# Kernel optimization log

Hardware: AMD Instinct MI355X
Metric: run time of the kernel (lower is better)

## Reference

```python
import jax, jax.numpy as jnp
import numpy as np

N_NODES = 50000


def gcn_conv(x, W, b, src, dst, num_nodes):
    """PyG GCNConv: add self-loops, symmetric deg^{-1/2} normalization,
    linear transform, scatter-add aggregation, bias."""
    loop = jnp.arange(num_nodes, dtype=src.dtype)
    s = jnp.concatenate([src, loop])  # message sources
    d = jnp.concatenate([dst, loop])  # message destinations
    deg = jax.ops.segment_sum(jnp.ones_like(d, dtype=x.dtype), d, num_segments=num_nodes)
    dinv = jnp.where(deg > 0, jax.lax.rsqrt(deg), 0.0)
    norm = dinv[s] * dinv[d]                      # [E+N]
    h = x @ W                                      # [N, out]
    msg = h[s] * norm[:, None]                     # gather + scale  [E+N, out]
    out = jax.ops.segment_sum(msg, d, num_segments=num_nodes)  # scatter-add
    return out + b


def setup_inputs() -> dict:
    key = jax.random.key(0)
    ks = jax.random.split(key, 8)
    n, e = N_NODES, 1600000
    d_in, d_h, d_out = 128, 128, 64
    x = jax.random.normal(ks[0], (n, d_in), dtype=jnp.float32)
    edge_index = jax.random.randint(ks[1], (2, e), 0, n, dtype=jnp.int32)
    s = 1.0 / np.sqrt(d_in)
    W1 = jax.random.uniform(ks[2], (d_in, d_h), jnp.float32, -s, s)
    b1 = jnp.zeros((d_h,), jnp.float32)
    W2 = jax.random.uniform(ks[3], (d_h, d_h), jnp.float32, -s, s)
    b2 = jnp.zeros((d_h,), jnp.float32)
    W3 = jax.random.uniform(ks[4], (d_h, d_out), jnp.float32, -s, s)
    b3 = jnp.zeros((d_out,), jnp.float32)
    return {"x": x, "edge_index": edge_index, "W1": W1, "b1": b1,
            "W2": W2, "b2": b2, "W3": W3, "b3": b3}


def reference(x, edge_index, W1, b1, W2, b2, W3, b3):
    src, dst = edge_index[0], edge_index[1]
    n = x.shape[0]
    # Dropout in eval mode (identity); ReLU between GCN layers.
    h = jax.nn.relu(gcn_conv(x, W1, b1, src, dst, n))
    h = jax.nn.relu(gcn_conv(h, W2, b2, src, dst, n))
    out = gcn_conv(h, W3, b3, src, dst, n)
    return out
```

## Files before the change

### kernel.cpp

```cpp
#include <hip/hip_runtime.h>
#include <type_traits>


#define EPB  4096
#define DIRW 197

typedef __attribute__((ext_vector_type(8))) short bf16x8;
typedef __attribute__((ext_vector_type(4))) float f32x4;
typedef __attribute__((ext_vector_type(2))) float f32x2;

__device__ __forceinline__ unsigned short f2bf(float f) {
    unsigned int u = __float_as_uint(f);
    u += 0x7FFFu + ((u >> 16) & 1u);
    return (unsigned short)(u >> 16);
}
__device__ __forceinline__ float bflo(unsigned int u) { return __uint_as_float(u << 16); }
__device__ __forceinline__ float bfhi(unsigned int u) { return __uint_as_float(u & 0xFFFF0000u); }

__global__ __launch_bounds__(256) void bin_kernel(const int* __restrict__ src,
                                                  const int* __restrict__ dst,
                                                  unsigned int* __restrict__ pair_buf,
                                                  int* __restrict__ dir,
                                                  int E, int nbkt) {
    __shared__ unsigned int stage[EPB];
    __shared__ int hist[DIRW];
    __shared__ int sc[256];
    __shared__ int cur[DIRW];
    int tid = threadIdx.x;
    int blk = blockIdx.x;
    if (tid < DIRW) hist[tid] = 0;
    __syncthreads();

    int s_reg[16], d_reg[16];
#pragma unroll
    for (int j = 0; j < 16; ++j) {
        int gi = blk * EPB + j * 256 + tid;
        int s = 0, d = nbkt << 8;
        if (gi < E) { s = src[gi]; d = dst[gi]; }
        s_reg[j] = s; d_reg[j] = d;
        atomicAdd(&hist[d >> 8], 1);
    }
    __syncthreads();
    int h = (tid < DIRW) ? hist[tid] : 0;
    sc[tid] = h;
    __syncthreads();
#pragma unroll
    for (int off = 1; off < 256; off <<= 1) {
        int v = (tid >= off) ? sc[tid - off] : 0;
        __syncthreads();
        sc[tid] += v;
        __syncthreads();
    }
    if (tid < DIRW) {
        int st = sc[tid] - h;
        cur[tid] = st;
        dir[blk * DIRW + tid] = st;
    }
    __syncthreads();
#pragma unroll
    for (int j = 0; j < 16; ++j) {
        int b = d_reg[j] >> 8;
        int slot = atomicAdd(&cur[b], 1);
        stage[slot] = ((unsigned int)s_reg[j] << 8) | (unsigned int)(d_reg[j] & 255);
    }
    __syncthreads();
#pragma unroll
    for (int j = 0; j < 16; ++j) {
        int idx = j * 256 + tid;
        pair_buf[blk * EPB + idx] = stage[idx];
    }
}

__global__ __launch_bounds__(512) void csr_sizes_kernel(const unsigned int* __restrict__ pair_buf,
                                                        const int* __restrict__ dir,
                                                        int* __restrict__ bucket_pad,
                                                        int NB) {
    __shared__ int dstart[400];
    __shared__ int dend[400];
    __shared__ int cnt[256];
    int tid = threadIdx.x;
    int b = blockIdx.x;
    for (int i = tid; i < NB; i += 512) {
        dstart[i] = dir[i * DIRW + b];
        dend[i]   = dir[i * DIRW + b + 1];
    }
    if (tid < 256) cnt[tid] = 0;
    __syncthreads();
    int wid = tid >> 6, lane = tid & 63;
    for (int seg = wid; seg < NB; seg += 8) {
        int s0 = dstart[seg], s1 = dend[seg];
        for (int k = s0 + lane; k < s1; k += 64) {
            unsigned int p = pair_buf[(size_t)seg * EPB + k];
            atomicAdd(&cnt[p & 255u], 1);
        }
    }
    __syncthreads();
    if (tid < 64) {
        int m = max(max(cnt[4 * tid], cnt[4 * tid + 1]),
                    max(cnt[4 * tid + 2], cnt[4 * tid + 3]));
        int L = (m + 7) & ~7;
        int s = L;
#pragma unroll
        for (int off = 1; off < 64; off <<= 1) s += __shfl_xor(s, off);
        if (tid == 0) bucket_pad[b] = 4 * s;
    }
}

__global__ __launch_bounds__(256) void bucket_scan_kernel(const int* __restrict__ bucket_pad,
                                                          int* __restrict__ bucket_base,
                                                          int* __restrict__ row_ptr,
                                                          int nbkt, int n) {
    __shared__ int sc[256];
    int tid = threadIdx.x;
    int h = (tid < nbkt) ? bucket_pad[tid] : 0;
    sc[tid] = h;
    __syncthreads();
#pragma unroll
    for (int off = 1; off < 256; off <<= 1) {
        int v = (tid >= off) ? sc[tid - off] : 0;
        __syncthreads();
        sc[tid] += v;
        __syncthreads();
    }
    if (tid <= nbkt) bucket_base[tid] = sc[tid] - h;
    if (tid == nbkt) row_ptr[n] = sc[tid] - h;
}

__global__ __launch_bounds__(512) void csr_place_kernel(const unsigned int* __restrict__ pair_buf,
                                                        const int* __restrict__ dir,
                                                        const int* __restrict__ bucket_base,
                                                        int* __restrict__ row_ptr,
                                                        float* __restrict__ dinv,
                                                        int* __restrict__ csr_src,
                                                        int n, int NB) {
    __shared__ int dstart[400];
    __shared__ int dend[400];
    __shared__ int cnt[256];
    __shared__ int Lg[64];
    __shared__ int Lpre[64];
    __shared__ int nbase[256];
    __shared__ int cur[256];
    int tid = threadIdx.x;
    int b = blockIdx.x;
    for (int i = tid; i < NB; i += 512) {
        dstart[i] = dir[i * DIRW + b];
        dend[i]   = dir[i * DIRW + b + 1];
    }
    if (tid < 256) cnt[tid] = 0;
    __syncthreads();
    int wid = tid >> 6, lane = tid & 63;
    for (int seg = wid; seg < NB; seg += 8) {
        int s0 = dstart[seg], s1 = dend[seg];
        for (int k = s0 + lane; k < s1; k += 64) {
            unsigned int p = pair_buf[(size_t)seg * EPB + k];
            atomicAdd(&cnt[p & 255u], 1);
        }
    }
    __syncthreads();
    if (tid < 64) {
        int m = max(max(cnt[4 * tid], cnt[4 * tid + 1]),
                    max(cnt[4 * tid + 2], cnt[4 * tid + 3]));
        int L = (m + 7) & ~7;
        int x = L;
#pragma unroll
        for (int off = 1; off < 64; off <<= 1) {
            int y = __shfl_up(x, off);
            if (tid >= off) x += y;
        }
        Lg[tid] = L;
        Lpre[tid] = x - L;
    }
    __syncthreads();
    int base = bucket_base[b];
    if (tid < 256) {
        int g = tid >> 2;
        int nb = base + 4 * Lpre[g] + (tid & 3) * Lg[g];
        nbase[tid] = nb;
        cur[tid] = nb;
        int d = b * 256 + tid;
        if (d < n) {
            row_ptr[d] = nb;
            dinv[d] = rsqrtf((float)(cnt[tid] + 1));
        }
    }
    __syncthreads();
    for (int seg = wid; seg < NB; seg += 8) {
        int s0 = dstart[seg], s1 = dend[seg];
        for (int k = s0 + lane; k < s1; k += 64) {
            unsigned int p = pair_buf[(size_t)seg * EPB + k];
            int pos = atomicAdd(&cur[p & 255u], 1);
            csr_src[pos] = (int)(p >> 8);
        }
    }
    __syncthreads();
    if (tid < 256) {
        int endp = nbase[tid] + Lg[tid >> 2];
        for (int pos = cur[tid]; pos < endp; ++pos) csr_src[pos] = n;
    }
}

template <int NOUT, typename TA, bool FP8OUT>
__global__ __launch_bounds__(256) void gemm_bf16_kernel(const TA* __restrict__ X,
                                                        const float* __restrict__ W,
                                                        const float* __restrict__ dinv,
                                                        void* __restrict__ Hout,
                                                        int n_rows) {
    __shared__ short As[64][132];
    __shared__ short Bs[NOUT][132];
    int tid = threadIdx.x;
    int row0 = blockIdx.x * 64;

    {
        int r = tid >> 2;
        int c0 = (tid & 3) * 32;
        int grow = row0 + r;
        if constexpr (std::is_same<TA, float>::value) {
            const float* xp = X + (size_t)grow * 128 + c0;
#pragma unroll
            for (int j = 0; j < 8; ++j) {
                float4 v = (grow < n_rows) ? *(const float4*)(xp + j * 4)
                                           : make_float4(0.f, 0.f, 0.f, 0.f);
                ushort4 p = { f2bf(v.x), f2bf(v.y), f2bf(v.z), f2bf(v.w) };
                *(ushort4*)&As[r][c0 + j * 4] = p;
            }
        } else {
            const unsigned short* xp = X + (size_t)grow * 128 + c0;
#pragma unroll
            for (int j = 0; j < 8; ++j) {
                uint2 v = (grow < n_rows) ? *(const uint2*)(xp + j * 4)
                                          : make_uint2(0u, 0u);
                *(uint2*)&As[r][c0 + j * 4] = v;
            }
        }
    }
    {
        int k = tid >> 1;
        int nb = (tid & 1) * (NOUT / 2);
        const float* wp = W + (size_t)k * NOUT + nb;
#pragma unroll
        for (int j = 0; j < NOUT / 8; ++j) {
            float4 v = *(const float4*)(wp + j * 4);
            int nn = nb + j * 4;
            Bs[nn + 0][k] = (short)f2bf(v.x);
            Bs[nn + 1][k] = (short)f2bf(v.y);
            Bs[nn + 2][k] = (short)f2bf(v.z);
            Bs[nn + 3][k] = (short)f2bf(v.w);
        }
    }
    __syncthreads();

    int w = tid >> 6, l = tid & 63, lr = l & 15, lg = l >> 4;
    constexpr int NF = NOUT / 16;
    f32x4 acc[NF];
#pragma unroll
    for (int i = 0; i < NF; ++i) acc[i] = (f32x4){0.f, 0.f, 0.f, 0.f};
    int arow = w * 16 + lr;

#pragma unroll
    for (int kc = 0; kc < 128; kc += 32) {
        bf16x8 a;
        ((long long*)&a)[0] = *(const long long*)&As[arow][kc + lg * 4];
        ((long long*)&a)[1] = *(const long long*)&As[arow][kc + 16 + lg * 4];
#pragma unroll
        for (int nf = 0; nf < NF; ++nf) {
            bf16x8 b;
            ((long long*)&b)[0] = *(const long long*)&Bs[nf * 16 + lr][kc + lg * 4];
            ((long long*)&b)[1] = *(const long long*)&Bs[nf * 16 + lr][kc + 16 + lg * 4];
            acc[nf] = __builtin_amdgcn_mfma_f32_16x16x32_bf16(a, b, acc[nf], 0, 0, 0);
        }
    }
    int grow_base = row0 + w * 16 + lg * 4;
    float dv[4];
#pragma unroll
    for (int r = 0; r < 4; ++r)
        dv[r] = (grow_base + r < n_rows) ? dinv[grow_base + r] : 0.f;
#pragma unroll
    for (int nf = 0; nf < NF; ++nf) {
#pragma unroll
        for (int r = 0; r < 4; ++r) {
            int gr = grow_base + r;
            if (gr < n_rows) {
                float val = acc[nf][r] * dv[r];
                if constexpr (FP8OUT) {
                    unsigned int pk = __builtin_amdgcn_cvt_pk_fp8_f32(val, val, 0, false);
                    ((unsigned char*)Hout)[(size_t)gr * NOUT + nf * 16 + lr] =
                        (unsigned char)(pk & 0xFFu);
                } else {
                    ((unsigned short*)Hout)[(size_t)gr * NOUT + nf * 16 + lr] = f2bf(val);
                }
            }
        }
    }
}

template <bool RELU>
__global__ __launch_bounds__(256) void agg128_kernel(const unsigned char* __restrict__ H,
                                                     const int* __restrict__ csr_src,
                                                     const int* __restrict__ row_ptr,
                                                     const float* __restrict__ dinv,
                                                     const float* __restrict__ bias,
                                                     unsigned short* __restrict__ out, int n) {
    int g = blockIdx.x * 4 + threadIdx.y;
    int node0 = g * 4;
    if (node0 >= n) return;
    int lane = threadIdx.x;
    int sub = lane >> 4, l16 = lane & 15;
    int node = node0 + sub;
    int base = row_ptr[node0];
    int L = (row_ptr[node0 + 4] - base) >> 2;
    int e0 = base + sub * L;
    const uint2* H2 = (const uint2*)H;
    float acc[8] = {0.f, 0.f, 0.f, 0.f, 0.f, 0.f, 0.f, 0.f};
    for (int k = 0; k < L; k += 8) {
        int idx[8];
#pragma unroll
        for (int j = 0; j < 8; ++j) idx[j] = csr_src[e0 + k + j];
        uint2 v[8];
#pragma unroll
        for (int j = 0; j < 8; ++j) v[j] = H2[(size_t)idx[j] * 16 + l16];
#pragma unroll
        for (int j = 0; j < 8; ++j) {
            f32x2 a0 = __builtin_amdgcn_cvt_pk_f32_fp8((int)v[j].x, false);
            f32x2 a1 = __builtin_amdgcn_cvt_pk_f32_fp8((int)v[j].x, true);
            f32x2 a2 = __builtin_amdgcn_cvt_pk_f32_fp8((int)v[j].y, false);
            f32x2 a3 = __builtin_amdgcn_cvt_pk_f32_fp8((int)v[j].y, true);
            acc[0] += a0.x; acc[1] += a0.y; acc[2] += a1.x; acc[3] += a1.y;
            acc[4] += a2.x; acc[5] += a2.y; acc[6] += a3.x; acc[7] += a3.y;
        }
    }
    uint2 vn = H2[(size_t)node * 16 + l16];
    {
        f32x2 a0 = __builtin_amdgcn_cvt_pk_f32_fp8((int)vn.x, false);
        f32x2 a1 = __builtin_amdgcn_cvt_pk_f32_fp8((int)vn.x, true);
        f32x2 a2 = __builtin_amdgcn_cvt_pk_f32_fp8((int)vn.y, false);
        f32x2 a3 = __builtin_amdgcn_cvt_pk_f32_fp8((int)vn.y, true);
        acc[0] += a0.x; acc[1] += a0.y; acc[2] += a1.x; acc[3] += a1.y;
        acc[4] += a2.x; acc[5] += a2.y; acc[6] += a3.x; acc[7] += a3.y;
    }
    float dn = dinv[node];
    const float4* b4 = (const float4*)(bias + l16 * 8);
    float4 bb0 = b4[0], bb1 = b4[1];
    float r0 = fmaf(acc[0], dn, bb0.x), r1 = fmaf(acc[1], dn, bb0.y);
    float r2 = fmaf(acc[2], dn, bb0.z), r3 = fmaf(acc[3], dn, bb0.w);
    float r4 = fmaf(acc[4], dn, bb1.x), r5 = fmaf(acc[5], dn, bb1.y);
    float r6 = fmaf(acc[6], dn, bb1.z), r7 = fmaf(acc[7], dn, bb1.w);
    if (RELU) {
        r0 = fmaxf(r0, 0.f); r1 = fmaxf(r1, 0.f); r2 = fmaxf(r2, 0.f); r3 = fmaxf(r3, 0.f);
        r4 = fmaxf(r4, 0.f); r5 = fmaxf(r5, 0.f); r6 = fmaxf(r6, 0.f); r7 = fmaxf(r7, 0.f);
    }
    uint4 pk;
    pk.x = ((unsigned int)f2bf(r1) << 16) | (unsigned int)f2bf(r0);
    pk.y = ((unsigned int)f2bf(r3) << 16) | (unsigned int)f2bf(r2);
    pk.z = ((unsigned int)f2bf(r5) << 16) | (unsigned int)f2bf(r4);
    pk.w = ((unsigned int)f2bf(r7) << 16) | (unsigned int)f2bf(r6);
    ((uint4*)out)[(size_t)node * 16 + l16] = pk;
}

__global__ __launch_bounds__(256) void agg64_kernel(const unsigned short* __restrict__ H,
                                                    const int* __restrict__ csr_src,
                                                    const int* __restrict__ row_ptr,
                                                    const float* __restrict__ dinv,
                                                    const float* __restrict__ bias,
                                                    float* __restrict__ out, int n) {
    int g = blockIdx.x * 4 + threadIdx.y;
    int node0 = g * 4;
    if (node0 >= n) return;
    int lane = threadIdx.x;
    int sub = lane >> 4, l16 = lane & 15;
    int node = node0 + sub;
    int base = row_ptr[node0];
    int L = (row_ptr[node0 + 4] - base) >> 2;
    int e0 = base + sub * L;
    const uint2* H2 = (const uint2*)H;
    float acc[4] = {0.f, 0.f, 0.f, 0.f};
    for (int k = 0; k < L; k += 8) {
        int idx[8];
#pragma unroll
        for (int j = 0; j < 8; ++j) idx[j] = csr_src[e0 + k + j];
        uint2 v[8];
#pragma unroll
        for (int j = 0; j < 8; ++j) v[j] = H2[(size_t)idx[j] * 16 + l16];
#pragma unroll
        for (int j = 0; j < 8; ++j) {
            acc[0] += bflo(v[j].x); acc[1] += bfhi(v[j].x);
            acc[2] += bflo(v[j].y); acc[3] += bfhi(v[j].y);
        }
    }
    uint2 vn = H2[(size_t)node * 16 + l16];
    acc[0] += bflo(vn.x); acc[1] += bfhi(vn.x);
    acc[2] += bflo(vn.y); acc[3] += bfhi(vn.y);
    float dn = dinv[node];
    float4 bb = *(const float4*)(bias + l16 * 4);
    float4 r;
    r.x = fmaf(acc[0], dn, bb.x);
    r.y = fmaf(acc[1], dn, bb.y);
    r.z = fmaf(acc[2], dn, bb.z);
    r.w = fmaf(acc[3], dn, bb.w);
    *(float4*)(out + (size_t)node * 64 + l16 * 4) = r;
}

extern "C" void kernel_launch(void* const* d_in, const int* in_sizes, int n_in,
                              void* d_out, int out_size, void* d_ws, size_t ws_size,
                              hipStream_t stream) {
    const float* x  = (const float*)d_in[0];
    const int*   ei = (const int*)d_in[1];
    const float* W1 = (const float*)d_in[2];
    const float* b1 = (const float*)d_in[3];
    const float* W2 = (const float*)d_in[4];
    const float* b2 = (const float*)d_in[5];
    const float* W3 = (const float*)d_in[6];
    const float* b3 = (const float*)d_in[7];

    const int n = in_sizes[0] / 128;
    const int E = in_sizes[1] / 2;
    const int* src = ei;
    const int* dst = ei + E;
    const int nbkt = (n + 255) >> 8;
    const int NB = (E + EPB - 1) / EPB;

    char* ws = (char*)d_ws;
    size_t off = 0;
    auto alloc = [&](size_t bytes) {
        void* p = ws + off;
        off = (off + bytes + 511) & ~(size_t)511;
        return p;
    };
    int*   bucket_pad  = (int*)alloc(256 * 4);
    int*   bucket_base = (int*)alloc(512 * 4);
    int*   row_ptr     = (int*)alloc((size_t)(n + 1) * 4);
    float* dinv        = (float*)alloc((size_t)n * 4);
    int*   csr_src     = (int*)alloc((size_t)4000000 * 4);
    unsigned char* Hb  = (unsigned char*)alloc((size_t)(n + 1) * 128);
    unsigned short* Bb = (unsigned short*)alloc((size_t)n * 128 * 2);
    unsigned int* pair_buf = (unsigned int*)Bb;
    int*          dir      = (int*)((char*)Bb + (size_t)NB * EPB * 4);
    (void)ws_size;

    bin_kernel<<<NB, 256, 0, stream>>>(src, dst, pair_buf, dir, E, nbkt);
    csr_sizes_kernel<<<nbkt, 512, 0, stream>>>(pair_buf, dir, bucket_pad, NB);
    bucket_scan_kernel<<<1, 256, 0, stream>>>(bucket_pad, bucket_base, row_ptr, nbkt, n);
    csr_place_kernel<<<nbkt, 512, 0, stream>>>(pair_buf, dir, bucket_base, row_ptr, dinv,
                                               csr_src, n, NB);
    hipMemsetAsync(Hb + (size_t)n * 128, 0, 128, stream);

    dim3 aggBlock(64, 4);
    int aggGrid = (n / 4 + 3) / 4;
    int gemmGrid = (n + 63) / 64;

    gemm_bf16_kernel<128, float, true><<<gemmGrid, 256, 0, stream>>>(x, W1, dinv, Hb, n);
    agg128_kernel<true><<<aggGrid, aggBlock, 0, stream>>>(Hb, csr_src, row_ptr, dinv, b1, Bb, n);
    gemm_bf16_kernel<128, unsigned short, true><<<gemmGrid, 256, 0, stream>>>(Bb, W2, dinv, Hb, n);
    agg128_kernel<true><<<aggGrid, aggBlock, 0, stream>>>(Hb, csr_src, row_ptr, dinv, b2, Bb, n);
    gemm_bf16_kernel<64, unsigned short, false><<<gemmGrid, 256, 0, stream>>>(Bb, W3, dinv, Hb, n);
    agg64_kernel<<<aggGrid, aggBlock, 0, stream>>>((unsigned short*)Hb, csr_src, row_ptr,
                                                   dinv, b3, (float*)d_out, n);
}
```

Measured before the change: 215.9 us.

## Reuse per-node counts in CSR placement and pre-transpose weights to bf16 once

csr_sizes now writes per-node in-degree counts and dinv to global memory, so csr_place no longer re-scans pair_buf with shared atomics to recount. The hipMemset of the padding row moves into bucket_scan_kernel. A new wtrans_kernel converts and transposes W1..W3 to bf16 once, so every GEMM block loads B with vector copies instead of converting and transposing per block with scattered LDS stores; the LDS row stride also changes to 136. This adds one small kernel launch and a global node_cnt buffer.

```diff
diff --git a/kernel.cpp b/kernel.cpp
--- a/kernel.cpp
+++ b/kernel.cpp
@@ -74,7 +74,9 @@
 __global__ __launch_bounds__(512) void csr_sizes_kernel(const unsigned int* __restrict__ pair_buf,
                                                         const int* __restrict__ dir,
                                                         int* __restrict__ bucket_pad,
-                                                        int NB) {
+                                                        int* __restrict__ node_cnt,
+                                                        float* __restrict__ dinv,
+                                                        int NB, int n) {
     __shared__ int dstart[400];
     __shared__ int dend[400];
     __shared__ int cnt[256];
@@ -95,6 +97,11 @@
         }
     }
     __syncthreads();
+    if (tid < 256) {
+        node_cnt[b * 256 + tid] = cnt[tid];
+        int d = b * 256 + tid;
+        if (d < n) dinv[d] = rsqrtf((float)(cnt[tid] + 1));
+    }
     if (tid < 64) {
         int m = max(max(cnt[4 * tid], cnt[4 * tid + 1]),
                     max(cnt[4 * tid + 2], cnt[4 * tid + 3]));
@@ -109,9 +116,11 @@
 __global__ __launch_bounds__(256) void bucket_scan_kernel(const int* __restrict__ bucket_pad,
                                                           int* __restrict__ bucket_base,
                                                           int* __restrict__ row_ptr,
+                                                          unsigned int* __restrict__ hb_pad_row,
                                                           int nbkt, int n) {
     __shared__ int sc[256];
     int tid = threadIdx.x;
+    if (tid < 32) hb_pad_row[tid] = 0u;
     int h = (tid < nbkt) ? bucket_pad[tid] : 0;
     sc[tid] = h;
     __syncthreads();
@@ -129,37 +138,30 @@
 __global__ __launch_bounds__(512) void csr_place_kernel(const unsigned int* __restrict__ pair_buf,
                                                         const int* __restrict__ dir,
                                                         const int* __restrict__ bucket_base,
+                                                        const int* __restrict__ node_cnt,
                                                         int* __restrict__ row_ptr,
-                                                        float* __restrict__ dinv,
                                                         int* __restrict__ csr_src,
                                                         int n, int NB) {
     __shared__ int dstart[400];
     __shared__ int dend[400];
-    __shared__ int cnt[256];
     __shared__ int Lg[64];
     __shared__ int Lpre[64];
     __shared__ int nbase[256];
     __shared__ int cur[256];
+    __shared__ int cend[256];
     int tid = threadIdx.x;
     int b = blockIdx.x;
     for (int i = tid; i < NB; i += 512) {
         dstart[i] = dir[i * DIRW + b];
         dend[i]   = dir[i * DIRW + b + 1];
     }
-    if (tid < 256) cnt[tid] = 0;
-    __syncthreads();
-    int wid = tid >> 6, lane = tid & 63;
-    for (int seg = wid; seg < NB; seg += 8) {
-        int s0 = dstart[seg], s1 = dend[seg];
-        for (int k = s0 + lane; k < s1; k += 64) {
-            unsigned int p = pair_buf[(size_t)seg * EPB + k];
-            atomicAdd(&cnt[p & 255u], 1);
-        }
-    }
     __syncthreads();
     if (tid < 64) {
-        int m = max(max(cnt[4 * tid], cnt[4 * tid + 1]),
-                    max(cnt[4 * tid + 2], cnt[4 * tid + 3]));
+        int c0 = node_cnt[b * 256 + 4 * tid + 0];
+        int c1 = node_cnt[b * 256 + 4 * tid + 1];
+        int c2 = node_cnt[b * 256 + 4 * tid + 2];
+        int c3 = node_cnt[b * 256 + 4 * tid + 3];
+        int m = max(max(c0, c1), max(c2, c3));
         int L = (m + 7) & ~7;
         int x = L;
 #pragma unroll
@@ -177,13 +179,12 @@
         int nb = base + 4 * Lpre[g] + (tid & 3) * Lg[g];
         nbase[tid] = nb;
         cur[tid] = nb;
+        cend[tid] = nb + Lg[g];
         int d = b * 256 + tid;
-        if (d < n) {
-            row_ptr[d] = nb;
-            dinv[d] = rsqrtf((float)(cnt[tid] + 1));
-        }
-    }
-    __syncthreads();
+        if (d < n) row_ptr[d] = nb;
+    }
+    __syncthreads();
+    int wid = tid >> 6, lane = tid & 63;
     for (int seg = wid; seg < NB; seg += 8) {
         int s0 = dstart[seg], s1 = dend[seg];
         for (int k = s0 + lane; k < s1; k += 64) {
@@ -194,19 +195,34 @@
     }
     __syncthreads();
     if (tid < 256) {
-        int endp = nbase[tid] + Lg[tid >> 2];
-        for (int pos = cur[tid]; pos < endp; ++pos) csr_src[pos] = n;
-    }
+        for (int pos = cur[tid]; pos < cend[tid]; ++pos) csr_src[pos] = n;
+    }
+}
+
+__global__ __launch_bounds__(256) void wtrans_kernel(const float* __restrict__ W1,
+                                                     const float* __restrict__ W2,
+                                                     const float* __restrict__ W3,
+                                                     unsigned short* __restrict__ Wt1,
+                                                     unsigned short* __restrict__ Wt2,
+                                                     unsigned short* __restrict__ Wt3) {
+    int blk = blockIdx.x;
+    const float* W; unsigned short* Wt; int N, e0;
+    if (blk < 64)       { W = W1; Wt = Wt1; N = 128; e0 = blk * 256; }
+    else if (blk < 128) { W = W2; Wt = Wt2; N = 128; e0 = (blk - 64) * 256; }
+    else                { W = W3; Wt = Wt3; N = 64;  e0 = (blk - 128) * 256; }
+    int e = e0 + threadIdx.x;
+    int nn = e >> 7, k = e & 127;
+    Wt[e] = f2bf(W[(size_t)k * N + nn]);
 }
 
 template <int NOUT, typename TA, bool FP8OUT>
 __global__ __launch_bounds__(256) void gemm_bf16_kernel(const TA* __restrict__ X,
-                                                        const float* __restrict__ W,
+                                                        const unsigned short* __restrict__ Wt,
                                                         const float* __restrict__ dinv,
                                                         void* __restrict__ Hout,
                                                         int n_rows) {
-    __shared__ short As[64][132];
-    __shared__ short Bs[NOUT][132];
+    __shared__ short As[64][136];
+    __shared__ short Bs[NOUT][136];
     int tid = threadIdx.x;
     int row0 = blockIdx.x * 64;
 
@@ -234,18 +250,14 @@
         }
     }
     {
-        int k = tid >> 1;
-        int nb = (tid & 1) * (NOUT / 2);
-        const float* wp = W + (size_t)k * NOUT + nb;
-#pragma unroll
-        for (int j = 0; j < NOUT / 8; ++j) {
-            float4 v = *(const float4*)(wp + j * 4);
-            int nn = nb + j * 4;
-            Bs[nn + 0][k] = (short)f2bf(v.x);
-            Bs[nn + 1][k] = (short)f2bf(v.y);
-            Bs[nn + 2][k] = (short)f2bf(v.z);
-            Bs[nn + 3][k] = (short)f2bf(v.w);
-        }
+        constexpr int TPR = 256 / NOUT;
+        constexpr int CH  = 128 / TPR;
+        int nrow = tid / TPR;
+        int seg  = tid % TPR;
+        const unsigned short* wp = Wt + (size_t)nrow * 128 + seg * CH;
+#pragma unroll
+        for (int j = 0; j < CH / 8; ++j)
+            *(uint4*)&Bs[nrow][seg * CH + j * 8] = *(const uint4*)(wp + j * 8);
     }
     __syncthreads();
 
@@ -429,7 +441,11 @@
     int*   bucket_base = (int*)alloc(512 * 4);
     int*   row_ptr     = (int*)alloc((size_t)(n + 1) * 4);
     float* dinv        = (float*)alloc((size_t)n * 4);
+    int*   node_cnt    = (int*)alloc((size_t)nbkt * 256 * 4);
     int*   csr_src     = (int*)alloc((size_t)4000000 * 4);
+    unsigned short* Wt1 = (unsigned short*)alloc(128 * 128 * 2);
+    unsigned short* Wt2 = (unsigned short*)alloc(128 * 128 * 2);
+    unsigned short* Wt3 = (unsigned short*)alloc(64 * 128 * 2);
     unsigned char* Hb  = (unsigned char*)alloc((size_t)(n + 1) * 128);
     unsigned short* Bb = (unsigned short*)alloc((size_t)n * 128 * 2);
     unsigned int* pair_buf = (unsigned int*)Bb;
@@ -437,21 +453,22 @@
     (void)ws_size;
 
     bin_kernel<<<NB, 256, 0, stream>>>(src, dst, pair_buf, dir, E, nbkt);
-    csr_sizes_kernel<<<nbkt, 512, 0, stream>>>(pair_buf, dir, bucket_pad, NB);
-    bucket_scan_kernel<<<1, 256, 0, stream>>>(bucket_pad, bucket_base, row_ptr, nbkt, n);
-    csr_place_kernel<<<nbkt, 512, 0, stream>>>(pair_buf, dir, bucket_base, row_ptr, dinv,
-                                               csr_src, n, NB);
-    hipMemsetAsync(Hb + (size_t)n * 128, 0, 128, stream);
+    csr_sizes_kernel<<<nbkt, 512, 0, stream>>>(pair_buf, dir, bucket_pad, node_cnt, dinv, NB, n);
+    bucket_scan_kernel<<<1, 256, 0, stream>>>(bucket_pad, bucket_base, row_ptr,
+                                              (unsigned int*)(Hb + (size_t)n * 128), nbkt, n);
+    csr_place_kernel<<<nbkt, 512, 0, stream>>>(pair_buf, dir, bucket_base, node_cnt,
+                                               row_ptr, csr_src, n, NB);
+    wtrans_kernel<<<160, 256, 0, stream>>>(W1, W2, W3, Wt1, Wt2, Wt3);
 
     dim3 aggBlock(64, 4);
     int aggGrid = (n / 4 + 3) / 4;
     int gemmGrid = (n + 63) / 64;
 
-    gemm_bf16_kernel<128, float, true><<<gemmGrid, 256, 0, stream>>>(x, W1, dinv, Hb, n);
+    gemm_bf16_kernel<128, float, true><<<gemmGrid, 256, 0, stream>>>(x, Wt1, dinv, Hb, n);
     agg128_kernel<true><<<aggGrid, aggBlock, 0, stream>>>(Hb, csr_src, row_ptr, dinv, b1, Bb, n);
-    gemm_bf16_kernel<128, unsigned short, true><<<gemmGrid, 256, 0, stream>>>(Bb, W2, dinv, Hb, n);
+    gemm_bf16_kernel<128, unsigned short, true><<<gemmGrid, 256, 0, stream>>>(Bb, Wt2, dinv, Hb, n);
     agg128_kernel<true><<<aggGrid, aggBlock, 0, stream>>>(Hb, csr_src, row_ptr, dinv, b2, Bb, n);
-    gemm_bf16_kernel<64, unsigned short, false><<<gemmGrid, 256, 0, stream>>>(Bb, W3, dinv, Hb, n);
+    gemm_bf16_kernel<64, unsigned short, false><<<gemmGrid, 256, 0, stream>>>(Bb, Wt3, dinv, Hb, n);
     agg64_kernel<<<aggGrid, aggBlock, 0, stream>>>((unsigned short*)Hb, csr_src, row_ptr,
                                                    dinv, b3, (float*)d_out, n);
 }
```

After: 198.7 us. -8.0%, faster.
